# Optimization experiments

Measured on AMD Instinct MI355X. Metric: run time of the kernel, lower is better.

The kernel has to match this reference:

```python
import jax, jax.numpy as jnp
import numpy as np

N = 1 << 20        # number of query points
L_HIDDEN = 6       # hidden (64->64) layers, i.e. params[1:-1]
NEG_SLOPE = 0.2    # nn.LeakyReLU(0.2)

# NOTE: nn.Dropout(0.5) is treated in eval mode (identity), the standard
# convention for deterministic correctness baselines.

def _lrelu(x):
    return jnp.where(x >= 0, x, NEG_SLOPE * x)


def setup_inputs() -> dict:
    key = jax.random.key(0)
    ks = jax.random.split(key, 11)
    return {
        "points": jax.random.normal(ks[0], (N, 3), jnp.float32),
        "w0": jax.random.normal(ks[1], (3, 64), jnp.float32),
        "s0": jax.random.normal(ks[2], (64,), jnp.float32),
        "b0": jax.random.normal(ks[3], (64,), jnp.float32),
        "wh": jax.random.normal(ks[4], (L_HIDDEN, 64, 64), jnp.float32),
        "sh": jax.random.normal(ks[5], (L_HIDDEN, 64), jnp.float32),
        "bh": jax.random.normal(ks[6], (L_HIDDEN, 64), jnp.float32),
        "wo": jax.random.normal(ks[7], (64, 1), jnp.float32),
        "so": jax.random.normal(ks[8], (), jnp.float32),
        "bo": jax.random.normal(ks[9], (), jnp.float32),
    }


def reference(points, w0, s0, b0, wh, sh, bh, wo, so, bo):
    # first layer: [N,3] @ [3,64] * scale + bias -> leakyrelu
    x = _lrelu(jnp.matmul(points, w0) * s0 + b0)
    # hidden layers: small static loop over structurally distinct param sets
    for i in range(L_HIDDEN):
        x = _lrelu(jnp.matmul(x, wh[i]) * sh[i] + bh[i])
    # output layer: [N,64] @ [64,1] * scalar + scalar (no activation)
    return jnp.matmul(x, wo) * so + bo
```

## Files before the change

kernel.cpp:

```cpp
#include <hip/hip_runtime.h>


typedef _Float16 half8 __attribute__((ext_vector_type(8)));
typedef _Float16 half2v __attribute__((ext_vector_type(2)));
typedef float floatx16 __attribute__((ext_vector_type(16)));

#define N_HID 6
#define OFF_A 0
#define OFF_B 49152
#define OFF_C 51200
#define OFF_D 52992
#define IMG_BYTES 53248
#define SETUP_TOTAL (24576 + 1024 + 448 + 64)

__global__ __launch_bounds__(256) void setup_weights(
    const float* __restrict__ w0, const float* __restrict__ s0, const float* __restrict__ b0,
    const float* __restrict__ wh, const float* __restrict__ sh, const float* __restrict__ bh,
    const float* __restrict__ wo, const float* __restrict__ so,
    unsigned char* __restrict__ ws)
{
    int i = blockIdx.x * 256 + threadIdx.x;
    if (i < 24576) {
        int j = i & 7, lane = (i >> 3) & 63, s = (i >> 9) & 3, t = (i >> 11) & 1, l = i >> 12;
        int m = 32 * t + (lane & 31);
        int h = lane >> 5;
        int feat = 16 * s + 8 * (j >> 2) + 4 * h + (j & 3);
        ((_Float16*)(ws + OFF_A))[i] = (_Float16)(wh[(l * 64 + feat) * 64 + m] * sh[l * 64 + m]);
    } else if (i < 24576 + 1024) {
        int i2 = i - 24576;
        int j = i2 & 7, lane = (i2 >> 3) & 63, t = i2 >> 9;
        int m = 32 * t + (lane & 31);
        int k = 8 * (lane >> 5) + j;
        float v = (k < 3) ? w0[k * 64 + m] * s0[m] * 0.015625f : 0.f;
        ((_Float16*)(ws + OFF_B))[i2] = (_Float16)v;
    } else if (i < 24576 + 1024 + 448) {
        int i2 = i - 24576 - 1024;
        int r = i2 & 15, t = (i2 >> 4) & 1, h = (i2 >> 5) & 1, l = i2 >> 6;
        int feat = 32 * t + (r & 3) + 8 * ((r >> 2) & 3) + 4 * h;
        float bv = (l == 0) ? b0[feat] : bh[(l - 1) * 64 + feat];
        ((float*)(ws + OFF_C))[i2] = bv * 0.015625f;
    } else if (i < SETUP_TOTAL) {
        int i2 = i - 24576 - 1024 - 448;
        int r = i2 & 15, t = (i2 >> 4) & 1, h = i2 >> 5;
        int feat = 32 * t + (r & 3) + 8 * ((r >> 2) & 3) + 4 * h;
        ((float*)(ws + OFF_D))[i2] = wo[feat] * so[0] * 64.f;
    }
}

union FragU { int i[4]; half8 v; };

static __device__ __forceinline__ int pkrtz(float a, float b) {
    auto hh = __builtin_amdgcn_cvt_pkrtz(a, b);
    int r;
    __builtin_memcpy(&r, &hh, 4);
    return r;
}

static __device__ __forceinline__ int lrelu2(int v) {
    half2v u;
    __builtin_memcpy(&u, &v, 4);
    half2v w = u * (_Float16)0.2f;
    half2v r = __builtin_elementwise_max(u, w);
    int o;
    __builtin_memcpy(&o, &r, 4);
    return o;
}

static __device__ __forceinline__ floatx16 mfma16(half8 a, half8 b, floatx16 c) {
    return __builtin_amdgcn_mfma_f32_32x32x16_f16(a, b, c, 0, 0, 0);
}

__global__ __launch_bounds__(256, 3) void mlp_mfma(
    const float* __restrict__ points,
    const unsigned char* __restrict__ ws,
    const float* __restrict__ bo,
    float* __restrict__ out, int n)
{
    __shared__ __align__(16) unsigned char lds[IMG_BYTES];

    {
        const uint4* src = (const uint4*)ws;
        uint4* dst = (uint4*)lds;
#pragma unroll
        for (int i = 0; i < 13; ++i) {
            int idx = threadIdx.x + 256 * i;
            dst[idx] = src[idx];
        }
    }
    __syncthreads();

    const int lane = threadIdx.x & 63;
    const int wv = threadIdx.x >> 6;
    const int p = lane & 31;
    const int h = lane >> 5;
    const int base = (blockIdx.x * 4 + wv) * 64;
    const int pt0 = base + p, pt1 = base + 32 + p;
    const int pl0 = min(pt0, n - 1), pl1 = min(pt1, n - 1);

    const half8* Wf = (const half8*)(lds + OFF_A);
    const half8* A0 = (const half8*)(lds + OFF_B);
    const floatx16* biasC = (const floatx16*)(lds + OFF_C);
    const floatx16* woC = (const floatx16*)(lds + OFF_D);

    floatx16 acc[2][2];
    int fr[2][16];

    {
        FragU bu0, bu1;
        bu0.i[0] = bu0.i[1] = bu0.i[2] = bu0.i[3] = 0;
        bu1 = bu0;
        if (h == 0) {
            bu0.v[0] = (_Float16)points[3 * pl0 + 0];
            bu0.v[1] = (_Float16)points[3 * pl0 + 1];
            bu0.v[2] = (_Float16)points[3 * pl0 + 2];
            bu1.v[0] = (_Float16)points[3 * pl1 + 0];
            bu1.v[1] = (_Float16)points[3 * pl1 + 1];
            bu1.v[2] = (_Float16)points[3 * pl1 + 2];
        }
        floatx16 c0 = biasC[h * 2 + 0];
        floatx16 c1 = biasC[h * 2 + 1];
        half8 a0 = A0[lane], a1 = A0[64 + lane];
        acc[0][0] = mfma16(a0, bu0.v, c0);
        acc[0][1] = mfma16(a1, bu0.v, c1);
        acc[1][0] = mfma16(a0, bu1.v, c0);
        acc[1][1] = mfma16(a1, bu1.v, c1);
    }

    auto packfr = [&]() {
#pragma unroll
        for (int nt = 0; nt < 2; ++nt)
#pragma unroll
            for (int t = 0; t < 2; ++t)
#pragma unroll
                for (int rp = 0; rp < 8; ++rp) {
                    int v = pkrtz(acc[nt][t][2 * rp], acc[nt][t][2 * rp + 1]);
                    fr[nt][8 * t + 2 * (rp >> 1) + (rp & 1)] = lrelu2(v);
                }
    };
    packfr();

    for (int l = 0; l < N_HID; ++l) {
        floatx16 c0 = biasC[((l + 1) * 2 + h) * 2 + 0];
        floatx16 c1 = biasC[((l + 1) * 2 + h) * 2 + 1];
        floatx16 a00 = c0, a01 = c1, a10 = c0, a11 = c1;
        const half8* wl = Wf + l * 512 + lane;
#pragma unroll
        for (int s = 0; s < 4; ++s) {
            half8 wt0 = wl[s * 64];
            half8 wt1 = wl[256 + s * 64];
            FragU f0, f1;
#pragma unroll
            for (int c = 0; c < 4; ++c) { f0.i[c] = fr[0][4 * s + c]; f1.i[c] = fr[1][4 * s + c]; }
            a00 = mfma16(wt0, f0.v, a00);
            a01 = mfma16(wt1, f0.v, a01);
            a10 = mfma16(wt0, f1.v, a10);
            a11 = mfma16(wt1, f1.v, a11);
        }
        acc[0][0] = a00; acc[0][1] = a01; acc[1][0] = a10; acc[1][1] = a11;
        if (l < N_HID - 1) packfr();
    }

    {
        floatx16 wo0 = woC[h * 2 + 0];
        floatx16 wo1 = woC[h * 2 + 1];
        float part0 = 0.f, part1 = 0.f;
#pragma unroll
        for (int r = 0; r < 16; ++r) {
            float u;
            u = acc[0][0][r]; part0 = fmaf(fmaxf(u, 0.2f * u), wo0[r], part0);
            u = acc[0][1][r]; part0 = fmaf(fmaxf(u, 0.2f * u), wo1[r], part0);
            u = acc[1][0][r]; part1 = fmaf(fmaxf(u, 0.2f * u), wo0[r], part1);
            u = acc[1][1][r]; part1 = fmaf(fmaxf(u, 0.2f * u), wo1[r], part1);
        }
        part0 += __shfl_xor(part0, 32);
        part1 += __shfl_xor(part1, 32);
        const float bov = bo[0];
        if (h == 0) {
            if (pt0 < n) out[pt0] = part0 + bov;
            if (pt1 < n) out[pt1] = part1 + bov;
        }
    }
}

extern "C" void kernel_launch(void* const* d_in, const int* in_sizes, int n_in,
                              void* d_out, int out_size, void* d_ws, size_t ws_size,
                              hipStream_t stream) {
    const float* points = (const float*)d_in[0];
    const float* w0     = (const float*)d_in[1];
    const float* s0     = (const float*)d_in[2];
    const float* b0     = (const float*)d_in[3];
    const float* wh     = (const float*)d_in[4];
    const float* sh     = (const float*)d_in[5];
    const float* bh     = (const float*)d_in[6];
    const float* wo     = (const float*)d_in[7];
    const float* so     = (const float*)d_in[8];
    const float* bo     = (const float*)d_in[9];

    const int n = in_sizes[0] / 3;

    setup_weights<<<(SETUP_TOTAL + 255) / 256, 256, 0, stream>>>(
        w0, s0, b0, wh, sh, bh, wo, so, (unsigned char*)d_ws);

    const int grid = (n + 255) / 256;
    mlp_mfma<<<grid, 256, 0, stream>>>(
        points, (const unsigned char*)d_ws, bo, (float*)d_out, n);
}
```

Before: 132.1 us.

## Hold all MLP weights in registers with persistent single-wave blocks

Replaces the per-block LDS weight staging with a persistent kernel: 1024 single-wave blocks load every hidden-layer weight fragment into registers once, then grid-stride over 64-point batches while prefetching the next batch's points. The first-layer bias is folded into the weight matrix through a constant-1 input, and hidden biases are produced by an extra MFMA against a one-hot fragment instead of being loaded from LDS. The output dot product is vectorised with packed float2 operations. This removes the repeated LDS fill, the barrier and the LDS reads, but it needs a very large register budget for the weights and limits occupancy to one wave per block, which may leave MFMA latency poorly hidden.

```diff
diff --git a/kernel.cpp b/kernel.cpp
--- a/kernel.cpp
+++ b/kernel.cpp
@@ -4,13 +4,13 @@
 typedef _Float16 half8 __attribute__((ext_vector_type(8)));
 typedef _Float16 half2v __attribute__((ext_vector_type(2)));
 typedef float floatx16 __attribute__((ext_vector_type(16)));
+typedef float float2v __attribute__((ext_vector_type(2)));
 
 #define N_HID 6
 #define OFF_A 0
 #define OFF_B 49152
 #define OFF_C 51200
 #define OFF_D 52992
-#define IMG_BYTES 53248
 #define SETUP_TOTAL (24576 + 1024 + 448 + 64)
 
 __global__ __launch_bounds__(256) void setup_weights(
@@ -31,7 +31,8 @@
         int j = i2 & 7, lane = (i2 >> 3) & 63, t = i2 >> 9;
         int m = 32 * t + (lane & 31);
         int k = 8 * (lane >> 5) + j;
-        float v = (k < 3) ? w0[k * 64 + m] * s0[m] * 0.015625f : 0.f;
+        float v = (k < 3) ? w0[k * 64 + m] * s0[m] * 0.015625f
+                          : (k == 3 ? b0[m] * 0.015625f : 0.f);
         ((_Float16*)(ws + OFF_B))[i2] = (_Float16)v;
     } else if (i < 24576 + 1024 + 448) {
         int i2 = i - 24576 - 1024;
@@ -70,115 +71,162 @@
     return __builtin_amdgcn_mfma_f32_32x32x16_f16(a, b, c, 0, 0, 0);
 }
 
-__global__ __launch_bounds__(256, 3) void mlp_mfma(
+__global__ __launch_bounds__(64, 1) void mlp_mfma(
     const float* __restrict__ points,
     const unsigned char* __restrict__ ws,
+    const float* __restrict__ bhg,
     const float* __restrict__ bo,
     float* __restrict__ out, int n)
 {
-    __shared__ __align__(16) unsigned char lds[IMG_BYTES];
-
-    {
-        const uint4* src = (const uint4*)ws;
-        uint4* dst = (uint4*)lds;
-#pragma unroll
-        for (int i = 0; i < 13; ++i) {
-            int idx = threadIdx.x + 256 * i;
-            dst[idx] = src[idx];
-        }
-    }
-    __syncthreads();
-
-    const int lane = threadIdx.x & 63;
-    const int wv = threadIdx.x >> 6;
+    const int lane = threadIdx.x;
     const int p = lane & 31;
     const int h = lane >> 5;
-    const int base = (blockIdx.x * 4 + wv) * 64;
-    const int pt0 = base + p, pt1 = base + 32 + p;
-    const int pl0 = min(pt0, n - 1), pl1 = min(pt1, n - 1);
-
-    const half8* Wf = (const half8*)(lds + OFF_A);
-    const half8* A0 = (const half8*)(lds + OFF_B);
-    const floatx16* biasC = (const floatx16*)(lds + OFF_C);
-    const floatx16* woC = (const floatx16*)(lds + OFF_D);
-
-    floatx16 acc[2][2];
-    int fr[2][16];
-
-    {
-        FragU bu0, bu1;
-        bu0.i[0] = bu0.i[1] = bu0.i[2] = bu0.i[3] = 0;
-        bu1 = bu0;
-        if (h == 0) {
-            bu0.v[0] = (_Float16)points[3 * pl0 + 0];
-            bu0.v[1] = (_Float16)points[3 * pl0 + 1];
-            bu0.v[2] = (_Float16)points[3 * pl0 + 2];
-            bu1.v[0] = (_Float16)points[3 * pl1 + 0];
-            bu1.v[1] = (_Float16)points[3 * pl1 + 1];
-            bu1.v[2] = (_Float16)points[3 * pl1 + 2];
-        }
-        floatx16 c0 = biasC[h * 2 + 0];
-        floatx16 c1 = biasC[h * 2 + 1];
-        half8 a0 = A0[lane], a1 = A0[64 + lane];
-        acc[0][0] = mfma16(a0, bu0.v, c0);
-        acc[0][1] = mfma16(a1, bu0.v, c1);
-        acc[1][0] = mfma16(a0, bu1.v, c0);
-        acc[1][1] = mfma16(a1, bu1.v, c1);
-    }
-
-    auto packfr = [&]() {
-#pragma unroll
-        for (int nt = 0; nt < 2; ++nt)
+
+    half8 Wreg[N_HID][2][4];
+    {
+        const half8* WfG = (const half8*)(ws + OFF_A);
+#pragma unroll
+        for (int l = 0; l < N_HID; ++l)
 #pragma unroll
             for (int t = 0; t < 2; ++t)
 #pragma unroll
-                for (int rp = 0; rp < 8; ++rp) {
-                    int v = pkrtz(acc[nt][t][2 * rp], acc[nt][t][2 * rp + 1]);
-                    fr[nt][8 * t + 2 * (rp >> 1) + (rp & 1)] = lrelu2(v);
+                for (int s = 0; s < 4; ++s)
+                    Wreg[l][t][s] = WfG[(((l * 2 + t) * 4 + s) << 6) + lane];
+    }
+    half8 W0a, W0b;
+    {
+        const half8* A0g = (const half8*)(ws + OFF_B);
+        W0a = A0g[lane];
+        W0b = A0g[64 + lane];
+    }
+    half8 biasF[N_HID][2];
+#pragma unroll
+    for (int l = 0; l < N_HID; ++l)
+#pragma unroll
+        for (int t = 0; t < 2; ++t) {
+            FragU u;
+            u.i[0] = u.i[1] = u.i[2] = u.i[3] = 0;
+            if (h == 0) u.v[0] = (_Float16)(bhg[l * 64 + 32 * t + p] * 0.015625f);
+            biasF[l][t] = u.v;
+        }
+    half8 oneF;
+    {
+        FragU u;
+        u.i[0] = u.i[1] = u.i[2] = u.i[3] = 0;
+        if (h == 0) u.v[0] = (_Float16)1.0f;
+        oneF = u.v;
+    }
+    floatx16 wo0, wo1;
+    {
+        const floatx16* woG = (const floatx16*)(ws + OFF_D);
+        wo0 = woG[h * 2 + 0];
+        wo1 = woG[h * 2 + 1];
+    }
+    const float bov = bo[0];
+
+    const int nbatch = (n + 63) >> 6;
+    int b = blockIdx.x;
+    if (b >= nbatch) return;
+
+    float P0x, P0y, P0z, P1x, P1y, P1z;
+    {
+        int q0 = min(b * 64 + p, n - 1), q1 = min(b * 64 + 32 + p, n - 1);
+        P0x = points[3 * q0]; P0y = points[3 * q0 + 1]; P0z = points[3 * q0 + 2];
+        P1x = points[3 * q1]; P1y = points[3 * q1 + 1]; P1z = points[3 * q1 + 2];
+    }
+
+    while (true) {
+        const int nb = b + (int)gridDim.x;
+        const bool more = nb < nbatch;
+        float N0x, N0y, N0z, N1x, N1y, N1z;
+        N0x = N0y = N0z = N1x = N1y = N1z = 0.f;
+        if (more) {
+            int q0 = min(nb * 64 + p, n - 1), q1 = min(nb * 64 + 32 + p, n - 1);
+            N0x = points[3 * q0]; N0y = points[3 * q0 + 1]; N0z = points[3 * q0 + 2];
+            N1x = points[3 * q1]; N1y = points[3 * q1 + 1]; N1z = points[3 * q1 + 2];
+        }
+
+        floatx16 acc0[2], acc1[2];
+        {
+            FragU bu0, bu1;
+            bu0.i[0] = bu0.i[1] = bu0.i[2] = bu0.i[3] = 0;
+            bu1 = bu0;
+            if (h == 0) {
+                bu0.v[0] = (_Float16)P0x; bu0.v[1] = (_Float16)P0y;
+                bu0.v[2] = (_Float16)P0z; bu0.v[3] = (_Float16)1.0f;
+                bu1.v[0] = (_Float16)P1x; bu1.v[1] = (_Float16)P1y;
+                bu1.v[2] = (_Float16)P1z; bu1.v[3] = (_Float16)1.0f;
+            }
+            acc0[0] = mfma16(W0a, bu0.v, (floatx16)(0.0f));
+            acc0[1] = mfma16(W0b, bu0.v, (floatx16)(0.0f));
+            acc1[0] = mfma16(W0a, bu1.v, (floatx16)(0.0f));
+            acc1[1] = mfma16(W0b, bu1.v, (floatx16)(0.0f));
+        }
+
+#pragma unroll
+        for (int l = 0; l < N_HID; ++l) {
+            floatx16 bc0 = mfma16(biasF[l][0], oneF, (floatx16)(0.0f));
+            floatx16 bc1 = mfma16(biasF[l][1], oneF, (floatx16)(0.0f));
+            floatx16 n00, n01, n10, n11;
+#pragma unroll
+            for (int s = 0; s < 4; ++s) {
+                const int t = s >> 1, rpb = 4 * (s & 1);
+                FragU f0, f1;
+#pragma unroll
+                for (int c = 0; c < 4; ++c) {
+                    f0.i[c] = lrelu2(pkrtz(acc0[t][2 * (rpb + c)], acc0[t][2 * (rpb + c) + 1]));
+                    f1.i[c] = lrelu2(pkrtz(acc1[t][2 * (rpb + c)], acc1[t][2 * (rpb + c) + 1]));
                 }
-    };
-    packfr();
-
-    for (int l = 0; l < N_HID; ++l) {
-        floatx16 c0 = biasC[((l + 1) * 2 + h) * 2 + 0];
-        floatx16 c1 = biasC[((l + 1) * 2 + h) * 2 + 1];
-        floatx16 a00 = c0, a01 = c1, a10 = c0, a11 = c1;
-        const half8* wl = Wf + l * 512 + lane;
-#pragma unroll
-        for (int s = 0; s < 4; ++s) {
-            half8 wt0 = wl[s * 64];
-            half8 wt1 = wl[256 + s * 64];
-            FragU f0, f1;
-#pragma unroll
-            for (int c = 0; c < 4; ++c) { f0.i[c] = fr[0][4 * s + c]; f1.i[c] = fr[1][4 * s + c]; }
-            a00 = mfma16(wt0, f0.v, a00);
-            a01 = mfma16(wt1, f0.v, a01);
-            a10 = mfma16(wt0, f1.v, a10);
-            a11 = mfma16(wt1, f1.v, a11);
-        }
-        acc[0][0] = a00; acc[0][1] = a01; acc[1][0] = a10; acc[1][1] = a11;
-        if (l < N_HID - 1) packfr();
-    }
-
-    {
-        floatx16 wo0 = woC[h * 2 + 0];
-        floatx16 wo1 = woC[h * 2 + 1];
-        float part0 = 0.f, part1 = 0.f;
-#pragma unroll
-        for (int r = 0; r < 16; ++r) {
-            float u;
-            u = acc[0][0][r]; part0 = fmaf(fmaxf(u, 0.2f * u), wo0[r], part0);
-            u = acc[0][1][r]; part0 = fmaf(fmaxf(u, 0.2f * u), wo1[r], part0);
-            u = acc[1][0][r]; part1 = fmaf(fmaxf(u, 0.2f * u), wo0[r], part1);
-            u = acc[1][1][r]; part1 = fmaf(fmaxf(u, 0.2f * u), wo1[r], part1);
-        }
-        part0 += __shfl_xor(part0, 32);
-        part1 += __shfl_xor(part1, 32);
-        const float bov = bo[0];
-        if (h == 0) {
-            if (pt0 < n) out[pt0] = part0 + bov;
-            if (pt1 < n) out[pt1] = part1 + bov;
-        }
+                if (s == 0) {
+                    n00 = mfma16(Wreg[l][0][0], f0.v, bc0);
+                    n01 = mfma16(Wreg[l][1][0], f0.v, bc1);
+                    n10 = mfma16(Wreg[l][0][0], f1.v, bc0);
+                    n11 = mfma16(Wreg[l][1][0], f1.v, bc1);
+                } else {
+                    n00 = mfma16(Wreg[l][0][s], f0.v, n00);
+                    n01 = mfma16(Wreg[l][1][s], f0.v, n01);
+                    n10 = mfma16(Wreg[l][0][s], f1.v, n10);
+                    n11 = mfma16(Wreg[l][1][s], f1.v, n11);
+                }
+            }
+            acc0[0] = n00; acc0[1] = n01; acc1[0] = n10; acc1[1] = n11;
+        }
+
+        {
+            float2v q0 = {0.f, 0.f}, q1 = {0.f, 0.f};
+#pragma unroll
+            for (int r2 = 0; r2 < 8; ++r2) {
+                float2v w0p = { wo0[2 * r2], wo0[2 * r2 + 1] };
+                float2v w1p = { wo1[2 * r2], wo1[2 * r2 + 1] };
+                float2v u;
+                u.x = acc0[0][2 * r2]; u.y = acc0[0][2 * r2 + 1];
+                u = __builtin_elementwise_max(u, 0.2f * u);
+                q0 += u * w0p;
+                u.x = acc0[1][2 * r2]; u.y = acc0[1][2 * r2 + 1];
+                u = __builtin_elementwise_max(u, 0.2f * u);
+                q0 += u * w1p;
+                u.x = acc1[0][2 * r2]; u.y = acc1[0][2 * r2 + 1];
+                u = __builtin_elementwise_max(u, 0.2f * u);
+                q1 += u * w0p;
+                u.x = acc1[1][2 * r2]; u.y = acc1[1][2 * r2 + 1];
+                u = __builtin_elementwise_max(u, 0.2f * u);
+                q1 += u * w1p;
+            }
+            float part0 = q0.x + q0.y;
+            float part1 = q1.x + q1.y;
+            part0 += __shfl_xor(part0, 32);
+            part1 += __shfl_xor(part1, 32);
+            if (h == 0) {
+                int pt0 = b * 64 + p, pt1 = b * 64 + 32 + p;
+                if (pt0 < n) out[pt0] = part0 + bov;
+                if (pt1 < n) out[pt1] = part1 + bov;
+            }
+        }
+
+        if (!more) break;
+        P0x = N0x; P0y = N0y; P0z = N0z;
+        P1x = N1x; P1y = N1y; P1z = N1z;
+        b = nb;
     }
 }
 
@@ -201,7 +249,6 @@
     setup_weights<<<(SETUP_TOTAL + 255) / 256, 256, 0, stream>>>(
         w0, s0, b0, wh, sh, bh, wo, so, (unsigned char*)d_ws);
 
-    const int grid = (n + 255) / 256;
-    mlp_mfma<<<grid, 256, 0, stream>>>(
-        points, (const unsigned char*)d_ws, bo, (float*)d_out, n);
-}
+    mlp_mfma<<<1024, 64, 0, stream>>>(
+        points, (const unsigned char*)d_ws, bh, bo, (float*)d_out, n);
+}
```

New measurement: 143.2 us. 1.08x slower.
